# Kernel optimization log

Hardware: AMD Instinct MI355X
Metric: run time of the kernel (lower is better)

The kernel has to match this reference:

```python
import jax, jax.numpy as jnp
import numpy as np

N = 100000   # nodes
E = 200000   # edges
L = 3        # GNN layers
D = 300      # node feature dim
H = 150      # per-direction message dim


def setup_inputs() -> dict:
    key = jax.random.key(0)
    ks = jax.random.split(key, 8)
    s = 0.05
    return {
        "x": jax.random.normal(ks[0], (N, D), jnp.float32),
        "edge_index": jax.random.randint(ks[1], (2, E), 0, N, dtype=jnp.int32),
        "Wr": jax.random.normal(ks[2], (L, 2 * D, H), jnp.float32) * s,
        "br": jax.random.normal(ks[3], (L, H), jnp.float32) * s,
        "Wc": jax.random.normal(ks[4], (L, 2 * D, H), jnp.float32) * s,
        "bc": jax.random.normal(ks[5], (L, H), jnp.float32) * s,
        "Wa": jax.random.normal(ks[6], (D, D), jnp.float32) * s,
        "ba": jax.random.normal(ks[7], (D,), jnp.float32) * s,
    }


def _gelu(z):
    return jax.nn.gelu(z, approximate=False)  # torch GELU is exact erf


def _msg_aggr(v, src, dst, W, b):
    # message at each edge: GELU(Linear(cat(x_i, x_j))), x_i = target, x_j = source
    m = _gelu(jnp.concatenate([v[dst], v[src]], axis=-1) @ W + b)  # [E, H]
    # sum-aggregate messages at target nodes
    return jax.ops.segment_sum(m, dst, num_segments=N)  # [N, H]


def reference(x, edge_index, Wr, br, Wc, bc, Wa, ba):
    src, dst = edge_index[0], edge_index[1]

    def step(v, p):
        Wr_l, br_l, Wc_l, bc_l = p
        r = _msg_aggr(v, src, dst, Wr_l, br_l)        # r2c: original direction
        c = _msg_aggr(v, dst, src, Wc_l, bc_l)        # c2r: flipped edge_index
        v = v + _gelu(jnp.concatenate([r, c], axis=-1) @ Wa + ba)
        return v, None

    out, _ = jax.lax.scan(step, x, (Wr, br, Wc, bc))
    return out
```

## Files before the change

kernel.cpp:

```cpp
#include <hip/hip_runtime.h>
#include <hip/hip_bf16.h>
#include <math.h>

#define NND 100000
#define EE  200000
#define LL  3
#define DD  300
#define HH  150

#define MPAD 100096
#define KP   320
#define NPJ  640
#define NUP  384
#define NTK  (KP / 32)

#define NB   49
#define SCN  (NB * 2048)

#define BSTRIDE 132

#define P_BR 0
#define P_BC 152
#define P_AR 304
#define P_AC 456
#define RC_R 0
#define RC_C 160

typedef __attribute__((ext_vector_type(8))) short bf16x8;
typedef __attribute__((ext_vector_type(4))) short bf16x4;
typedef __attribute__((ext_vector_type(4))) float f32x4;

__device__ __forceinline__ float gelu_exact(float z) {
    return 0.5f * z * (1.0f + erff(z * 0.7071067811865475f));
}
__device__ __forceinline__ unsigned short f2bf(float f) {
    union { float fv; unsigned u; } v; v.fv = f;
    unsigned r = v.u + 0x7fff + ((v.u >> 16) & 1);
    return (unsigned short)(r >> 16);
}
__device__ __forceinline__ float bf2f(unsigned short b) {
    union { unsigned u; float fv; } v; v.u = ((unsigned)b) << 16;
    return v.fv;
}

__global__ __launch_bounds__(256) void pack_w(
    const float* __restrict__ Wr, const float* __restrict__ Wc,
    const float* __restrict__ Wa,
    unsigned short* __restrict__ Bt, unsigned short* __restrict__ Wat)
{
    int i = blockIdx.x * 256 + threadIdx.x;
    const int btTotal = LL * NPJ * KP;
    if (i < btTotal) {
        int l = i / (NPJ * KP);
        int rem = i % (NPJ * KP);
        int n = rem / KP;
        int k = rem % KP;
        float v = 0.f;
        if (k < DD) {
            const float* W = nullptr; int krow = k, j = -1;
            if (n >= P_BR && n < P_BR + 150)      { W = Wr; krow = 300 + k; j = n - P_BR; }
            else if (n >= P_BC && n < P_BC + 150) { W = Wc; krow = 300 + k; j = n - P_BC; }
            else if (n >= P_AR && n < P_AR + 150) { W = Wr; krow = k;       j = n - P_AR; }
            else if (n >= P_AC && n < P_AC + 150) { W = Wc; krow = k;       j = n - P_AC; }
            if (j >= 0)
                v = W[(size_t)l * 600 * 150 + (size_t)krow * 150 + j];
        }
        Bt[i] = f2bf(v);
    } else {
        int i2 = i - btTotal;
        if (i2 < NUP * KP) {
            int n = i2 / KP, k = i2 % KP;
            int kk = -1;
            if (k < 150)                 kk = k;
            else if (k >= 160 && k < 310) kk = k - 10;
            float v = (n < DD && kk >= 0) ? Wa[(size_t)kk * DD + n] : 0.f;
            Wat[i2] = f2bf(v);
        }
    }
}

__global__ __launch_bounds__(256) void init_vbf(
    const float* __restrict__ x, unsigned short* __restrict__ vbf)
{
    int idx = blockIdx.x * 256 + threadIdx.x;
    int row = idx / (KP / 8);
    int gk  = (idx % (KP / 8)) * 8;
    if (row >= MPAD) return;
    unsigned short tmp[8];
    if (row < NND && gk < DD) {
        if (gk + 8 <= DD) {
            const float4* p = (const float4*)(x + (size_t)row * DD + gk);
            float4 f0 = p[0], f1 = p[1];
            tmp[0] = f2bf(f0.x); tmp[1] = f2bf(f0.y);
            tmp[2] = f2bf(f0.z); tmp[3] = f2bf(f0.w);
            tmp[4] = f2bf(f1.x); tmp[5] = f2bf(f1.y);
            tmp[6] = f2bf(f1.z); tmp[7] = f2bf(f1.w);
        } else {
            #pragma unroll
            for (int j = 0; j < 8; ++j)
                tmp[j] = (gk + j < DD) ? f2bf(x[(size_t)row * DD + gk + j]) : 0;
        }
    } else {
        #pragma unroll
        for (int j = 0; j < 8; ++j) tmp[j] = 0;
    }
    *((bf16x8*)&vbf[(size_t)row * KP + gk]) = *((bf16x8*)tmp);
}

__global__ __launch_bounds__(256) void hist_deg(
    const int* __restrict__ src, const int* __restrict__ dst,
    int* __restrict__ deg)
{
    int e = blockIdx.x * 256 + threadIdx.x;
    if (e >= EE) return;
    atomicAdd(&deg[dst[e]], 1);
    atomicAdd(&deg[SCN + src[e]], 1);
}

__global__ __launch_bounds__(256) void scanA(
    const int* __restrict__ deg, int* __restrict__ off, int* __restrict__ bsum)
{
    __shared__ int ls[256];
    const int t = threadIdx.x, row = blockIdx.y;
    const int base = blockIdx.x * 2048 + t * 8;
    const int* dg = deg + (size_t)row * SCN + base;
    int v[8];
    #pragma unroll
    for (int j = 0; j < 8; ++j) v[j] = dg[j];
    int tot = 0;
    #pragma unroll
    for (int j = 0; j < 8; ++j) tot += v[j];
    ls[t] = tot;
    __syncthreads();
    #pragma unroll
    for (int d = 1; d < 256; d <<= 1) {
        int tv = (t >= d) ? ls[t - d] : 0;
        __syncthreads();
        ls[t] += tv;
        __syncthreads();
    }
    int run = ls[t] - tot;
    int* op = off + (size_t)row * SCN + base;
    #pragma unroll
    for (int j = 0; j < 8; ++j) { op[j] = run; run += v[j]; }
    if (t == 255) bsum[row * 64 + blockIdx.x] = ls[255];
}

__global__ __launch_bounds__(256) void scanB(int* __restrict__ bsum)
{
    if (threadIdx.x < 2) {
        int row = threadIdx.x, c = 0;
        for (int i = 0; i < NB; ++i) {
            int tv = bsum[row * 64 + i];
            bsum[row * 64 + i] = c;
            c += tv;
        }
    }
}

__global__ __launch_bounds__(256) void scanC(
    int* __restrict__ off, const int* __restrict__ bsum, int* __restrict__ cur)
{
    const int t = threadIdx.x, row = blockIdx.y;
    const int base = blockIdx.x * 2048 + t * 8;
    const int add = bsum[row * 64 + blockIdx.x];
    int* op = off + (size_t)row * SCN + base;
    int* cp = cur + (size_t)row * SCN + base;
    #pragma unroll
    for (int j = 0; j < 8; ++j) {
        int v = op[j] + add;
        op[j] = v;
        cp[j] = v;
    }
}

__global__ __launch_bounds__(256) void fill_adj(
    const int* __restrict__ src, const int* __restrict__ dst,
    int* __restrict__ cur, int* __restrict__ adj)
{
    int e = blockIdx.x * 256 + threadIdx.x;
    if (e >= EE) return;
    int s = src[e], d = dst[e];
    int pd = atomicAdd(&cur[d], 1);
    adj[pd] = s;
    int ps = atomicAdd(&cur[SCN + s], 1);
    adj[EE + ps] = d;
}

__global__ __launch_bounds__(256) void aggregate(
    const int* __restrict__ off, const int* __restrict__ adj,
    const unsigned short* __restrict__ P,
    const float* __restrict__ br, const float* __restrict__ bc,
    unsigned short* __restrict__ RC)
{
    const int n    = blockIdx.x * 4 + (threadIdx.x >> 6);
    const int dir  = blockIdx.y;
    const int lane = threadIdx.x & 63;
    const int c    = lane * 4;

    if (lane < 10)
        RC[(size_t)n * KP + (dir ? 310 : 150) + lane] = 0;
    if (c >= 152) return;

    const int* offp = off + (size_t)dir * SCN;
    const int* adjp = adj + (size_t)dir * EE;
    const float* bias = dir ? bc : br;
    const unsigned short* own = P + (size_t)n * NPJ + (dir ? P_AC : P_AR);
    const int poff = dir ? P_BC : P_BR;

    const bool g0 = (c + 0) < 150, g1 = (c + 1) < 150;
    const bool g2 = (c + 2) < 150, g3 = (c + 3) < 150;

    bf16x4 ow = *((const bf16x4*)&own[c]);
    float o0 = bf2f((unsigned short)ow[0]) + (g0 ? bias[c + 0] : 0.f);
    float o1 = bf2f((unsigned short)ow[1]) + (g1 ? bias[c + 1] : 0.f);
    float o2 = bf2f((unsigned short)ow[2]) + (g2 ? bias[c + 2] : 0.f);
    float o3 = bf2f((unsigned short)ow[3]) + (g3 ? bias[c + 3] : 0.f);

    float s0 = 0.f, s1 = 0.f, s2 = 0.f, s3 = 0.f;
    int beg = offp[n], end = offp[n + 1];
    if (beg < end) {
        int a = adjp[beg];
        for (int i = beg; i < end; ++i) {
            int anext = (i + 1 < end) ? adjp[i + 1] : 0;
            const unsigned short* pp = P + (size_t)a * NPJ + poff;
            bf16x4 pv = *((const bf16x4*)&pp[c]);
            s0 += gelu_exact(o0 + bf2f((unsigned short)pv[0]));
            s1 += gelu_exact(o1 + bf2f((unsigned short)pv[1]));
            s2 += gelu_exact(o2 + bf2f((unsigned short)pv[2]));
            s3 += gelu_exact(o3 + bf2f((unsigned short)pv[3]));
            a = anext;
        }
    }
    unsigned short* outrow = RC + (size_t)n * KP + (dir ? RC_C : RC_R);
    if (c + 4 <= 150) {
        bf16x4 o;
        o[0] = (short)f2bf(s0); o[1] = (short)f2bf(s1);
        o[2] = (short)f2bf(s2); o[3] = (short)f2bf(s3);
        *((bf16x4*)&outrow[c]) = o;
    } else {
        if (g0) outrow[c + 0] = f2bf(s0);
        if (g1) outrow[c + 1] = f2bf(s1);
    }
}

#define GLOAD16(gp, lp) __builtin_amdgcn_global_load_lds( \
    (const __attribute__((address_space(1))) unsigned int*)(gp), \
    (__attribute__((address_space(3))) unsigned int*)(lp), 16, 0, 0)

#define STAGE_LDS(dstp, srcbase, rowoff, k0) do {                            \
    _Pragma("unroll")                                                        \
    for (int i_ = 0; i_ < 2; ++i_) {                                         \
        int cb_ = wid * 128 + i_ * 64;                                       \
        int ci_ = cb_ + lane;                                                \
        int row_ = ci_ >> 2, pc_ = ci_ & 3;                                  \
        int c_ = pc_ ^ ((row_ >> 1) & 3);                                    \
        GLOAD16(srcbase + (size_t)(rowoff + row_) * KP + (k0) + c_ * 8,      \
                &(dstp)[cb_ * 8]);                                           \
    } } while (0)

template<int MODE>
__global__ __launch_bounds__(256) void gemm_mfma(
    const unsigned short* __restrict__ Ab,
    const unsigned short* __restrict__ Bt,
    unsigned short* __restrict__ P,
    float* __restrict__ outv, unsigned short* __restrict__ vbf,
    const float* __restrict__ bias, int last)
{
    __shared__ char smem[4 * 16384];
    float* bounce = (float*)smem;

    const int tid  = threadIdx.x;
    const int lane = tid & 63;
    const int wid  = tid >> 6;

    const int gx   = gridDim.x;
    const int nwg  = gx * gridDim.y;
    const int flat = blockIdx.y * gx + blockIdx.x;
    const int q = nwg >> 3, r = nwg & 7;
    const int xcd = flat & 7, off = flat >> 3;
    const int lid = (xcd < r ? xcd * (q + 1) : r * (q + 1) + (xcd - r) * q) + off;
    const int brow = (lid / gx) * 128;
    const int bcol = (lid % gx) * 128;

    const int wm = (wid >> 1) * 64;
    const int wn = (wid & 1) * 64;

    f32x4 acc[4][4];
    #pragma unroll
    for (int i = 0; i < 4; ++i)
        #pragma unroll
        for (int j = 0; j < 4; ++j)
            #pragma unroll
            for (int rr = 0; rr < 4; ++rr) acc[i][j][rr] = 0.f;

    #pragma unroll
    for (int t = 0; t < 3; ++t) {
        unsigned short* Al = (unsigned short*)(smem + t * 16384);
        unsigned short* Bl = (unsigned short*)(smem + t * 16384 + 8192);
        STAGE_LDS(Al, Ab, brow, t * 32);
        STAGE_LDS(Bl, Bt, bcol, t * 32);
    }

    #pragma unroll
    for (int t = 0; t < NTK; ++t) {
        const int b = t & 3;
        unsigned short* Alc = (unsigned short*)(smem + b * 16384);
        unsigned short* Blc = (unsigned short*)(smem + b * 16384 + 8192);
        if (t <= NTK - 3) {
            asm volatile("s_waitcnt vmcnt(8)" ::: "memory");
        } else if (t == NTK - 2) {
            asm volatile("s_waitcnt vmcnt(4)" ::: "memory");
        } else {
            asm volatile("s_waitcnt vmcnt(0)" ::: "memory");
        }
        __builtin_amdgcn_s_barrier();
        if (t + 3 < NTK) {
            const int bn = (t + 3) & 3;
            unsigned short* Aln = (unsigned short*)(smem + bn * 16384);
            unsigned short* Bln = (unsigned short*)(smem + bn * 16384 + 8192);
            STAGE_LDS(Aln, Ab, brow, (t + 3) * 32);
            STAGE_LDS(Bln, Bt, bcol, (t + 3) * 32);
        }

        bf16x8 af[4], bfr[4];
        #pragma unroll
        for (int mi = 0; mi < 4; ++mi) {
            int row = wm + mi * 16 + (lane & 15);
            af[mi] = *((const bf16x8*)&Alc[row * 32 + (((lane >> 4) ^ ((row >> 1) & 3)) * 8)]);
        }
        #pragma unroll
        for (int nj = 0; nj < 4; ++nj) {
            int row = wn + nj * 16 + (lane & 15);
            bfr[nj] = *((const bf16x8*)&Blc[row * 32 + (((lane >> 4) ^ ((row >> 1) & 3)) * 8)]);
        }
        __builtin_amdgcn_s_setprio(1);
        #pragma unroll
        for (int mi = 0; mi < 4; ++mi)
            #pragma unroll
            for (int nj = 0; nj < 4; ++nj)
                acc[mi][nj] = __builtin_amdgcn_mfma_f32_16x16x32_bf16(
                    af[mi], bfr[nj], acc[mi][nj], 0, 0, 0);
        __builtin_amdgcn_s_setprio(0);
    }
    __builtin_amdgcn_s_barrier();

    const int ro = tid >> 5;
    const int co = (tid & 31) * 4;
    #pragma unroll
    for (int half = 0; half < 2; ++half) {
        if (wm == half * 64) {
            #pragma unroll
            for (int mi = 0; mi < 4; ++mi)
                #pragma unroll
                for (int nj = 0; nj < 4; ++nj) {
                    int lcol = wn + nj * 16 + (lane & 15);
                    int rb = mi * 16 + ((lane >> 4) << 2);
                    #pragma unroll
                    for (int rr = 0; rr < 4; ++rr)
                        bounce[(rb + rr) * BSTRIDE + lcol] = acc[mi][nj][rr];
                }
        }
        __syncthreads();
        #pragma unroll
        for (int i = 0; i < 8; ++i) {
            int lrow = ro + i * 8;
            int grow = brow + half * 64 + lrow;
            float4 vv = *(const float4*)&bounce[lrow * BSTRIDE + co];
            if (MODE == 0) {
                bf16x4 o;
                o[0] = (short)f2bf(vv.x); o[1] = (short)f2bf(vv.y);
                o[2] = (short)f2bf(vv.z); o[3] = (short)f2bf(vv.w);
                *((bf16x4*)&P[(size_t)grow * NPJ + bcol + co]) = o;
            } else if (grow < NND) {
                int gc = bcol + co;
                if (bcol < 256) {
                    float4 bv = *(const float4*)&bias[gc];
                    bf16x4 old = *(const bf16x4*)&vbf[(size_t)grow * KP + gc];
                    float4 nv;
                    nv.x = bf2f((unsigned short)old[0]) + gelu_exact(vv.x + bv.x);
                    nv.y = bf2f((unsigned short)old[1]) + gelu_exact(vv.y + bv.y);
                    nv.z = bf2f((unsigned short)old[2]) + gelu_exact(vv.z + bv.z);
                    nv.w = bf2f((unsigned short)old[3]) + gelu_exact(vv.w + bv.w);
                    if (last) {
                        *((float4*)&outv[(size_t)grow * DD + gc]) = nv;
                    } else {
                        bf16x4 o;
                        o[0] = (short)f2bf(nv.x); o[1] = (short)f2bf(nv.y);
                        o[2] = (short)f2bf(nv.z); o[3] = (short)f2bf(nv.w);
                        *((bf16x4*)&vbf[(size_t)grow * KP + gc]) = o;
                    }
                } else {
                    #pragma unroll
                    for (int j = 0; j < 4; ++j) {
                        int ccc = gc + j;
                        if (ccc < DD) {
                            float vj = (j == 0) ? vv.x : (j == 1) ? vv.y
                                     : (j == 2) ? vv.z : vv.w;
                            size_t vidx = (size_t)grow * KP + ccc;
                            float nv = bf2f(vbf[vidx]) + gelu_exact(vj + bias[ccc]);
                            if (last) outv[(size_t)grow * DD + ccc] = nv;
                            else      vbf[vidx] = f2bf(nv);
                        }
                    }
                }
            }
        }
        __syncthreads();
    }
}

extern "C" void kernel_launch(void* const* d_in, const int* in_sizes, int n_in,
                              void* d_out, int out_size, void* d_ws, size_t ws_size,
                              hipStream_t stream) {
    const float* x  = (const float*)d_in[0];
    const int*   ei = (const int*)  d_in[1];
    const float* Wr = (const float*)d_in[2];
    const float* br = (const float*)d_in[3];
    const float* Wc = (const float*)d_in[4];
    const float* bc = (const float*)d_in[5];
    const float* Wa = (const float*)d_in[6];
    const float* ba = (const float*)d_in[7];
    float* out = (float*)d_out;

    const size_t P_elems   = (size_t)MPAD * NPJ;
    const size_t RC_elems  = (size_t)MPAD * KP;
    const size_t V_elems   = (size_t)MPAD * KP;
    const size_t Bt_elems  = (size_t)LL * NPJ * KP;
    const size_t Wat_elems = (size_t)NUP * KP;

    unsigned short* P   = (unsigned short*)d_ws;
    unsigned short* RC  = P + P_elems;
    unsigned short* vbf = RC + RC_elems;
    unsigned short* Bt  = vbf + V_elems;
    unsigned short* Wat = Bt + Bt_elems;
    int* deg  = (int*)(Wat + Wat_elems);
    int* off  = deg + 2 * SCN;
    int* curp = off + 2 * SCN;
    int* adj  = curp + 2 * SCN;
    int* bsum = adj + 2 * EE;
    const size_t need = (char*)(bsum + 128) - (char*)d_ws;
    if (ws_size < need) return;

    pack_w<<<2880, 256, 0, stream>>>(Wr, Wc, Wa, Bt, Wat);
    init_vbf<<<(int)((V_elems / 8 + 255) / 256), 256, 0, stream>>>(x, vbf);

    const int* src = ei;
    const int* dst = ei + EE;

    hipMemsetAsync(deg, 0, 2 * SCN * sizeof(int), stream);
    hist_deg<<<(EE + 255) / 256, 256, 0, stream>>>(src, dst, deg);
    scanA<<<dim3(NB, 2), 256, 0, stream>>>(deg, off, bsum);
    scanB<<<1, 256, 0, stream>>>(bsum);
    scanC<<<dim3(NB, 2), 256, 0, stream>>>(off, bsum, curp);
    fill_adj<<<(EE + 255) / 256, 256, 0, stream>>>(src, dst, curp, adj);

    dim3 gproj(NPJ / 128, MPAD / 128);
    dim3 gupd (NUP / 128, MPAD / 128);
    dim3 gagg (MPAD / 4, 2);

    for (int l = 0; l < LL; ++l) {
        gemm_mfma<0><<<gproj, 256, 0, stream>>>(
            vbf, Bt + (size_t)l * NPJ * KP, P, nullptr, nullptr, nullptr, 0);
        aggregate<<<gagg, 256, 0, stream>>>(
            off, adj, P, br + (size_t)l * HH, bc + (size_t)l * HH, RC);
        gemm_mfma<1><<<gupd, 256, 0, stream>>>(
            RC, Wat, nullptr, out, vbf, ba, (l == LL - 1) ? 1 : 0);
    }
}
```

Measured before the change: 954.9 us.

## Keep full-K B fragments in registers and shrink GEMM M-tile to 64

The GEMM kernel now preloads each wave's whole K-extent of weight (B) fragments into registers up front and streams only the A tile through LDS, with a 4-deep LDS ring of single 16-byte loads per thread. The block tile shrinks from 128x128 to 64x128, each wave covering 64x32, which doubles the grid and cuts LDS use. The goal is to remove B staging and LDS reads from the inner loop and raise occupancy. In exchange it needs many more VGPRs for the B fragments (10x2 bf16x8), gets less A reuse per block, and re-reads B from global memory in twice as many blocks.

Measured after the change: 1.038 ms. 1.09x slower.

```diff
diff --git a/kernel.cpp b/kernel.cpp
--- a/kernel.cpp
+++ b/kernel.cpp
@@ -248,26 +248,16 @@
     (const __attribute__((address_space(1))) unsigned int*)(gp), \
     (__attribute__((address_space(3))) unsigned int*)(lp), 16, 0, 0)
 
-#define STAGE_LDS(dstp, srcbase, rowoff, k0) do {                            \
-    _Pragma("unroll")                                                        \
-    for (int i_ = 0; i_ < 2; ++i_) {                                         \
-        int cb_ = wid * 128 + i_ * 64;                                       \
-        int ci_ = cb_ + lane;                                                \
-        int row_ = ci_ >> 2, pc_ = ci_ & 3;                                  \
-        int c_ = pc_ ^ ((row_ >> 1) & 3);                                    \
-        GLOAD16(srcbase + (size_t)(rowoff + row_) * KP + (k0) + c_ * 8,      \
-                &(dstp)[cb_ * 8]);                                           \
-    } } while (0)
-
 template<int MODE>
-__global__ __launch_bounds__(256) void gemm_mfma(
+__global__ __launch_bounds__(256) void gemm_breg(
     const unsigned short* __restrict__ Ab,
     const unsigned short* __restrict__ Bt,
     unsigned short* __restrict__ P,
     float* __restrict__ outv, unsigned short* __restrict__ vbf,
     const float* __restrict__ bias, int last)
 {
-    __shared__ char smem[4 * 16384];
+    __shared__ char smem[64 * BSTRIDE * 4];
+    unsigned short* Alds = (unsigned short*)smem;
     float* bounce = (float*)smem;
 
     const int tid  = threadIdx.x;
@@ -280,133 +270,124 @@
     const int q = nwg >> 3, r = nwg & 7;
     const int xcd = flat & 7, off = flat >> 3;
     const int lid = (xcd < r ? xcd * (q + 1) : r * (q + 1) + (xcd - r) * q) + off;
-    const int brow = (lid / gx) * 128;
+    const int brow = (lid / gx) * 64;
     const int bcol = (lid % gx) * 128;
 
-    const int wm = (wid >> 1) * 64;
-    const int wn = (wid & 1) * 64;
-
-    f32x4 acc[4][4];
+    const int wn = wid * 32;
+
+    f32x4 acc[4][2];
     #pragma unroll
     for (int i = 0; i < 4; ++i)
         #pragma unroll
-        for (int j = 0; j < 4; ++j)
+        for (int j = 0; j < 2; ++j)
             #pragma unroll
             for (int rr = 0; rr < 4; ++rr) acc[i][j][rr] = 0.f;
 
-    #pragma unroll
-    for (int t = 0; t < 3; ++t) {
-        unsigned short* Al = (unsigned short*)(smem + t * 16384);
-        unsigned short* Bl = (unsigned short*)(smem + t * 16384 + 8192);
-        STAGE_LDS(Al, Ab, brow, t * 32);
-        STAGE_LDS(Bl, Bt, bcol, t * 32);
-    }
-
+    bf16x8 bfr[NTK][2];
+    const unsigned short* Bb =
+        Bt + (size_t)(bcol + wn + (lane & 15)) * KP + (lane >> 4) * 8;
     #pragma unroll
     for (int t = 0; t < NTK; ++t) {
-        const int b = t & 3;
-        unsigned short* Alc = (unsigned short*)(smem + b * 16384);
-        unsigned short* Blc = (unsigned short*)(smem + b * 16384 + 8192);
-        if (t <= NTK - 3) {
-            asm volatile("s_waitcnt vmcnt(8)" ::: "memory");
-        } else if (t == NTK - 2) {
-            asm volatile("s_waitcnt vmcnt(4)" ::: "memory");
+        bfr[t][0] = *((const bf16x8*)(Bb + t * 32));
+        bfr[t][1] = *((const bf16x8*)(Bb + (size_t)16 * KP + t * 32));
+    }
+
+    const int arow = tid >> 2;
+    const int ac   = (tid & 3) ^ ((arow >> 1) & 3);
+    const unsigned short* asrc = Ab + (size_t)(brow + arow) * KP + ac * 8;
+
+    #pragma unroll
+    for (int t = 0; t < 3; ++t)
+        GLOAD16(asrc + t * 32, Alds + t * 2048 + wid * 512);
+
+    #pragma unroll
+    for (int t = 0; t < NTK; ++t) {
+        unsigned short* Alc = Alds + (t & 3) * 2048;
+        if (t + 2 < NTK) {
+            asm volatile("s_waitcnt vmcnt(2)" ::: "memory");
+        } else if (t + 1 < NTK) {
+            asm volatile("s_waitcnt vmcnt(1)" ::: "memory");
         } else {
             asm volatile("s_waitcnt vmcnt(0)" ::: "memory");
         }
         __builtin_amdgcn_s_barrier();
-        if (t + 3 < NTK) {
-            const int bn = (t + 3) & 3;
-            unsigned short* Aln = (unsigned short*)(smem + bn * 16384);
-            unsigned short* Bln = (unsigned short*)(smem + bn * 16384 + 8192);
-            STAGE_LDS(Aln, Ab, brow, (t + 3) * 32);
-            STAGE_LDS(Bln, Bt, bcol, (t + 3) * 32);
-        }
-
-        bf16x8 af[4], bfr[4];
+        if (t + 3 < NTK)
+            GLOAD16(asrc + (t + 3) * 32, Alds + ((t + 3) & 3) * 2048 + wid * 512);
+
+        bf16x8 af[4];
         #pragma unroll
         for (int mi = 0; mi < 4; ++mi) {
-            int row = wm + mi * 16 + (lane & 15);
+            int row = mi * 16 + (lane & 15);
             af[mi] = *((const bf16x8*)&Alc[row * 32 + (((lane >> 4) ^ ((row >> 1) & 3)) * 8)]);
-        }
-        #pragma unroll
-        for (int nj = 0; nj < 4; ++nj) {
-            int row = wn + nj * 16 + (lane & 15);
-            bfr[nj] = *((const bf16x8*)&Blc[row * 32 + (((lane >> 4) ^ ((row >> 1) & 3)) * 8)]);
         }
         __builtin_amdgcn_s_setprio(1);
         #pragma unroll
         for (int mi = 0; mi < 4; ++mi)
             #pragma unroll
-            for (int nj = 0; nj < 4; ++nj)
+            for (int nj = 0; nj < 2; ++nj)
                 acc[mi][nj] = __builtin_amdgcn_mfma_f32_16x16x32_bf16(
-                    af[mi], bfr[nj], acc[mi][nj], 0, 0, 0);
+                    af[mi], bfr[t][nj], acc[mi][nj], 0, 0, 0);
         __builtin_amdgcn_s_setprio(0);
     }
-    __builtin_amdgcn_s_barrier();
+    __syncthreads();
+
+    #pragma unroll
+    for (int mi = 0; mi < 4; ++mi)
+        #pragma unroll
+        for (int nj = 0; nj < 2; ++nj) {
+            int lcol = wn + nj * 16 + (lane & 15);
+            int rb = mi * 16 + ((lane >> 4) << 2);
+            #pragma unroll
+            for (int rr = 0; rr < 4; ++rr)
+                bounce[(rb + rr) * BSTRIDE + lcol] = acc[mi][nj][rr];
+        }
+    __syncthreads();
 
     const int ro = tid >> 5;
     const int co = (tid & 31) * 4;
     #pragma unroll
-    for (int half = 0; half < 2; ++half) {
-        if (wm == half * 64) {
-            #pragma unroll
-            for (int mi = 0; mi < 4; ++mi)
+    for (int i = 0; i < 8; ++i) {
+        int lrow = ro + i * 8;
+        int grow = brow + lrow;
+        float4 vv = *(const float4*)&bounce[lrow * BSTRIDE + co];
+        if (MODE == 0) {
+            bf16x4 o;
+            o[0] = (short)f2bf(vv.x); o[1] = (short)f2bf(vv.y);
+            o[2] = (short)f2bf(vv.z); o[3] = (short)f2bf(vv.w);
+            *((bf16x4*)&P[(size_t)grow * NPJ + bcol + co]) = o;
+        } else if (grow < NND) {
+            int gc = bcol + co;
+            if (bcol < 256) {
+                float4 bv = *(const float4*)&bias[gc];
+                bf16x4 old = *(const bf16x4*)&vbf[(size_t)grow * KP + gc];
+                float4 nv;
+                nv.x = bf2f((unsigned short)old[0]) + gelu_exact(vv.x + bv.x);
+                nv.y = bf2f((unsigned short)old[1]) + gelu_exact(vv.y + bv.y);
+                nv.z = bf2f((unsigned short)old[2]) + gelu_exact(vv.z + bv.z);
+                nv.w = bf2f((unsigned short)old[3]) + gelu_exact(vv.w + bv.w);
+                if (last) {
+                    *((float4*)&outv[(size_t)grow * DD + gc]) = nv;
+                } else {
+                    bf16x4 o;
+                    o[0] = (short)f2bf(nv.x); o[1] = (short)f2bf(nv.y);
+                    o[2] = (short)f2bf(nv.z); o[3] = (short)f2bf(nv.w);
+                    *((bf16x4*)&vbf[(size_t)grow * KP + gc]) = o;
+                }
+            } else {
                 #pragma unroll
-                for (int nj = 0; nj < 4; ++nj) {
-                    int lcol = wn + nj * 16 + (lane & 15);
-                    int rb = mi * 16 + ((lane >> 4) << 2);
-                    #pragma unroll
-                    for (int rr = 0; rr < 4; ++rr)
-                        bounce[(rb + rr) * BSTRIDE + lcol] = acc[mi][nj][rr];
-                }
-        }
-        __syncthreads();
-        #pragma unroll
-        for (int i = 0; i < 8; ++i) {
-            int lrow = ro + i * 8;
-            int grow = brow + half * 64 + lrow;
-            float4 vv = *(const float4*)&bounce[lrow * BSTRIDE + co];
-            if (MODE == 0) {
-                bf16x4 o;
-                o[0] = (short)f2bf(vv.x); o[1] = (short)f2bf(vv.y);
-                o[2] = (short)f2bf(vv.z); o[3] = (short)f2bf(vv.w);
-                *((bf16x4*)&P[(size_t)grow * NPJ + bcol + co]) = o;
-            } else if (grow < NND) {
-                int gc = bcol + co;
-                if (bcol < 256) {
-                    float4 bv = *(const float4*)&bias[gc];
-                    bf16x4 old = *(const bf16x4*)&vbf[(size_t)grow * KP + gc];
-                    float4 nv;
-                    nv.x = bf2f((unsigned short)old[0]) + gelu_exact(vv.x + bv.x);
-                    nv.y = bf2f((unsigned short)old[1]) + gelu_exact(vv.y + bv.y);
-                    nv.z = bf2f((unsigned short)old[2]) + gelu_exact(vv.z + bv.z);
-                    nv.w = bf2f((unsigned short)old[3]) + gelu_exact(vv.w + bv.w);
-                    if (last) {
-                        *((float4*)&outv[(size_t)grow * DD + gc]) = nv;
-                    } else {
-                        bf16x4 o;
-                        o[0] = (short)f2bf(nv.x); o[1] = (short)f2bf(nv.y);
-                        o[2] = (short)f2bf(nv.z); o[3] = (short)f2bf(nv.w);
-                        *((bf16x4*)&vbf[(size_t)grow * KP + gc]) = o;
-                    }
-                } else {
-                    #pragma unroll
-                    for (int j = 0; j < 4; ++j) {
-                        int ccc = gc + j;
-                        if (ccc < DD) {
-                            float vj = (j == 0) ? vv.x : (j == 1) ? vv.y
-                                     : (j == 2) ? vv.z : vv.w;
-                            size_t vidx = (size_t)grow * KP + ccc;
-                            float nv = bf2f(vbf[vidx]) + gelu_exact(vj + bias[ccc]);
-                            if (last) outv[(size_t)grow * DD + ccc] = nv;
-                            else      vbf[vidx] = f2bf(nv);
-                        }
+                for (int j = 0; j < 4; ++j) {
+                    int ccc = gc + j;
+                    if (ccc < DD) {
+                        float vj = (j == 0) ? vv.x : (j == 1) ? vv.y
+                                 : (j == 2) ? vv.z : vv.w;
+                        size_t vidx = (size_t)grow * KP + ccc;
+                        float nv = bf2f(vbf[vidx]) + gelu_exact(vj + bias[ccc]);
+                        if (last) outv[(size_t)grow * DD + ccc] = nv;
+                        else      vbf[vidx] = f2bf(nv);
                     }
                 }
             }
         }
-        __syncthreads();
     }
 }
 
@@ -455,16 +436,16 @@
     scanC<<<dim3(NB, 2), 256, 0, stream>>>(off, bsum, curp);
     fill_adj<<<(EE + 255) / 256, 256, 0, stream>>>(src, dst, curp, adj);
 
-    dim3 gproj(NPJ / 128, MPAD / 128);
-    dim3 gupd (NUP / 128, MPAD / 128);
+    dim3 gproj(NPJ / 128, MPAD / 64);
+    dim3 gupd (NUP / 128, MPAD / 64);
     dim3 gagg (MPAD / 4, 2);
 
     for (int l = 0; l < LL; ++l) {
-        gemm_mfma<0><<<gproj, 256, 0, stream>>>(
+        gemm_breg<0><<<gproj, 256, 0, stream>>>(
             vbf, Bt + (size_t)l * NPJ * KP, P, nullptr, nullptr, nullptr, 0);
         aggregate<<<gagg, 256, 0, stream>>>(
             off, adj, P, br + (size_t)l * HH, bc + (size_t)l * HH, RC);
-        gemm_mfma<1><<<gupd, 256, 0, stream>>>(
+        gemm_breg<1><<<gupd, 256, 0, stream>>>(
             RC, Wat, nullptr, out, vbf, ba, (l == LL - 1) ? 1 : 0);
     }
 }
```

## Add register-resident B projection GEMM with 64-row tiles and A-only LDS pipeline

Applied to the files above, without the earlier changes.

Replaces the projection GEMM with a dedicated kernel that loads each wave's whole slice of B (all K for its 32 columns) into registers once. Only A tiles are staged in LDS, through a 4-slot ring of global-to-LDS loads with hand-placed waitcnt and barriers. Tiles drop to 64 rows, which doubles the grid and cuts LDS use so more workgroups fit per CU. The update GEMM becomes a non-template kernel. This trades higher register pressure and repeated B reads per tile for less LDS traffic and more occupancy.

After: 1.052 ms. 1.1x slower.

```diff
diff --git a/kernel.cpp b/kernel.cpp
--- a/kernel.cpp
+++ b/kernel.cpp
@@ -248,6 +248,117 @@
     (const __attribute__((address_space(1))) unsigned int*)(gp), \
     (__attribute__((address_space(3))) unsigned int*)(lp), 16, 0, 0)
 
+__global__ __launch_bounds__(256) void gemm_breg(
+    const unsigned short* __restrict__ Ab,
+    const unsigned short* __restrict__ Bt,
+    unsigned short* __restrict__ P)
+{
+    __shared__ char smem[16896];
+    unsigned short* Alds = (unsigned short*)smem;
+    float* bounce = (float*)smem;
+
+    const int tid  = threadIdx.x;
+    const int lane = tid & 63;
+    const int wid  = tid >> 6;
+
+    const int gx   = gridDim.x;
+    const int nwg  = gx * gridDim.y;
+    const int flat = blockIdx.y * gx + blockIdx.x;
+    const int q = nwg >> 3, r = nwg & 7;
+    const int xcd = flat & 7, off = flat >> 3;
+    const int lid = (xcd < r ? xcd * (q + 1) : r * (q + 1) + (xcd - r) * q) + off;
+    const int brow = (lid / gx) * 64;
+    const int bcol = (lid % gx) * 128;
+
+    const int wn = wid * 32;
+
+    f32x4 acc[4][2];
+    #pragma unroll
+    for (int i = 0; i < 4; ++i)
+        #pragma unroll
+        for (int j = 0; j < 2; ++j)
+            #pragma unroll
+            for (int rr = 0; rr < 4; ++rr) acc[i][j][rr] = 0.f;
+
+    bf16x8 bfr[NTK][2];
+    const unsigned short* Bb =
+        Bt + (size_t)(bcol + wn + (lane & 15)) * KP + (lane >> 4) * 8;
+    #pragma unroll
+    for (int t = 0; t < NTK; ++t) {
+        bfr[t][0] = *((const bf16x8*)(Bb + t * 32));
+        bfr[t][1] = *((const bf16x8*)(Bb + (size_t)16 * KP + t * 32));
+    }
+
+    const int arow = tid >> 2;
+    const int ac   = (tid & 3) ^ ((arow >> 1) & 3);
+    const unsigned short* asrc = Ab + (size_t)(brow + arow) * KP + ac * 8;
+
+    #pragma unroll
+    for (int t = 0; t < 3; ++t)
+        GLOAD16(asrc + t * 32, Alds + t * 2048 + wid * 512);
+
+    #pragma unroll
+    for (int t = 0; t < NTK; ++t) {
+        unsigned short* Alc = Alds + (t & 3) * 2048;
+        if (t + 2 < NTK) {
+            asm volatile("s_waitcnt vmcnt(2)" ::: "memory");
+        } else if (t + 1 < NTK) {
+            asm volatile("s_waitcnt vmcnt(1)" ::: "memory");
+        } else {
+            asm volatile("s_waitcnt vmcnt(0)" ::: "memory");
+        }
+        __builtin_amdgcn_s_barrier();
+        if (t + 3 < NTK)
+            GLOAD16(asrc + (t + 3) * 32, Alds + ((t + 3) & 3) * 2048 + wid * 512);
+
+        bf16x8 af[4];
+        #pragma unroll
+        for (int mi = 0; mi < 4; ++mi) {
+            int row = mi * 16 + (lane & 15);
+            af[mi] = *((const bf16x8*)&Alc[row * 32 + (((lane >> 4) ^ ((row >> 1) & 3)) * 8)]);
+        }
+        __builtin_amdgcn_s_setprio(1);
+        #pragma unroll
+        for (int mi = 0; mi < 4; ++mi)
+            #pragma unroll
+            for (int nj = 0; nj < 2; ++nj)
+                acc[mi][nj] = __builtin_amdgcn_mfma_f32_16x16x32_bf16(
+                    af[mi], bfr[t][nj], acc[mi][nj], 0, 0, 0);
+        __builtin_amdgcn_s_setprio(0);
+    }
+    __syncthreads();
+
+    const int ro = tid >> 5;
+    const int co = (tid & 31) * 4;
+    #pragma unroll
+    for (int half = 0; half < 2; ++half) {
+        #pragma unroll
+        for (int mi2 = 0; mi2 < 2; ++mi2) {
+            int mi = half * 2 + mi2;
+            #pragma unroll
+            for (int nj = 0; nj < 2; ++nj) {
+                int lcol = wn + nj * 16 + (lane & 15);
+                int rb = mi2 * 16 + ((lane >> 4) << 2);
+                #pragma unroll
+                for (int rr = 0; rr < 4; ++rr)
+                    bounce[(rb + rr) * BSTRIDE + lcol] = acc[mi][nj][rr];
+            }
+        }
+        __syncthreads();
+        #pragma unroll
+        for (int i = 0; i < 4; ++i) {
+            int lrow = ro + i * 8;
+            int grow = brow + half * 32 + lrow;
+            float4 vv = *(const float4*)&bounce[lrow * BSTRIDE + co];
+            bf16x4 o;
+            o[0] = (short)f2bf(vv.x); o[1] = (short)f2bf(vv.y);
+            o[2] = (short)f2bf(vv.z); o[3] = (short)f2bf(vv.w);
+            *((bf16x4*)&P[(size_t)grow * NPJ + bcol + co]) = o;
+        }
+        __syncthreads();
+    }
+}
+
 #define STAGE_LDS(dstp, srcbase, rowoff, k0) do {                            \
     _Pragma("unroll")                                                        \
     for (int i_ = 0; i_ < 2; ++i_) {                                         \
@@ -259,11 +370,9 @@
                 &(dstp)[cb_ * 8]);                                           \
     } } while (0)
 
-template<int MODE>
-__global__ __launch_bounds__(256) void gemm_mfma(
+__global__ __launch_bounds__(256) void gemm_upd(
     const unsigned short* __restrict__ Ab,
     const unsigned short* __restrict__ Bt,
-    unsigned short* __restrict__ P,
     float* __restrict__ outv, unsigned short* __restrict__ vbf,
     const float* __restrict__ bias, int last)
 {
@@ -367,12 +476,7 @@
             int lrow = ro + i * 8;
             int grow = brow + half * 64 + lrow;
             float4 vv = *(const float4*)&bounce[lrow * BSTRIDE + co];
-            if (MODE == 0) {
-                bf16x4 o;
-                o[0] = (short)f2bf(vv.x); o[1] = (short)f2bf(vv.y);
-                o[2] = (short)f2bf(vv.z); o[3] = (short)f2bf(vv.w);
-                *((bf16x4*)&P[(size_t)grow * NPJ + bcol + co]) = o;
-            } else if (grow < NND) {
+            if (grow < NND) {
                 int gc = bcol + co;
                 if (bcol < 256) {
                     float4 bv = *(const float4*)&bias[gc];
@@ -455,16 +559,16 @@
     scanC<<<dim3(NB, 2), 256, 0, stream>>>(off, bsum, curp);
     fill_adj<<<(EE + 255) / 256, 256, 0, stream>>>(src, dst, curp, adj);
 
-    dim3 gproj(NPJ / 128, MPAD / 128);
+    dim3 gproj(NPJ / 128, MPAD / 64);
     dim3 gupd (NUP / 128, MPAD / 128);
     dim3 gagg (MPAD / 4, 2);
 
     for (int l = 0; l < LL; ++l) {
-        gemm_mfma<0><<<gproj, 256, 0, stream>>>(
-            vbf, Bt + (size_t)l * NPJ * KP, P, nullptr, nullptr, nullptr, 0);
+        gemm_breg<<<gproj, 256, 0, stream>>>(
+            vbf, Bt + (size_t)l * NPJ * KP, P);
         aggregate<<<gagg, 256, 0, stream>>>(
             off, adj, P, br + (size_t)l * HH, bc + (size_t)l * HH, RC);
-        gemm_mfma<1><<<gupd, 256, 0, stream>>>(
-            RC, Wat, nullptr, out, vbf, ba, (l == LL - 1) ? 1 : 0);
-    }
-}
+        gemm_upd<<<gupd, 256, 0, stream>>>(
+            RC, Wat, out, vbf, ba, (l == LL - 1) ? 1 : 0);
+    }
+}
```
